# Kernel optimization log

Hardware: AMD Instinct MI355X
Metric: run time of the kernel (lower is better)

Reference implementation:

```python
import jax, jax.numpy as jnp
import numpy as np

N_NODES = 4096
EDGE_PROB = 0.01


def setup_inputs() -> dict:
    key = jax.random.key(0)
    kx, ka, kw = jax.random.split(key, 3)
    x = jax.random.normal(kx, (4, 32, N_NODES, 12), dtype=jnp.float32)
    u = jax.random.uniform(ka, (N_NODES, N_NODES), dtype=jnp.float32)
    adj = (u < EDGE_PROB).astype(jnp.float32)
    adj = jnp.maximum(adj, adj.T)
    weight = jax.random.normal(kw, (3, 32, 32), dtype=jnp.float32) * 0.1
    bias = jnp.zeros((32,), dtype=jnp.float32)
    return {"x": x, "adj": adj, "weight": weight, "bias": bias}


def reference(x, adj, weight, bias):
    # x: [B, c_in, N, T] -> [B, T, N, c_in] as in AdaptiveGraphConv.forward
    B, C, N, T = x.shape
    h = jnp.transpose(x, (0, 3, 2, 1))  # [B, T, N, C]
    # DenseChebConv (K=3): L = I - D^{-1/2} A D^{-1/2}, inf -> 0 for isolated nodes
    d = adj.sum(axis=-1)
    d_inv_sqrt = jnp.where(d > 0, jnp.where(d > 0, d, 1.0) ** -0.5, 0.0)
    norm_adj = d_inv_sqrt[:, None] * adj * d_inv_sqrt[None, :]
    L = jnp.eye(N, dtype=x.dtype) - norm_adj
    Tx0 = h
    Tx1 = jnp.einsum('mn,btnc->btmc', L, h)
    Tx2 = 2.0 * jnp.einsum('mn,btnc->btmc', L, Tx1) - Tx0
    out = (jnp.einsum('btnc,co->btno', Tx0, weight[0])
           + jnp.einsum('btnc,co->btno', Tx1, weight[1])
           + jnp.einsum('btnc,co->btno', Tx2, weight[2])
           + bias)
    # back to [B, c_out, N, T]
    return jnp.transpose(out, (0, 3, 2, 1))
```

## Files before the change

### kernel.cpp

```cpp
#include <hip/hip_runtime.h>

#define NN 4096
#define CC 32
#define TT 12
#define BB 4
#define BT 48
#define NC 1536
#define MAXD 192
#define FW 512
#define NCH 3
#define STP 36
#define SOP 33

typedef float f32x4 __attribute__((ext_vector_type(4)));
typedef short short8 __attribute__((ext_vector_type(8)));
typedef unsigned short ushort8 __attribute__((ext_vector_type(8)));

__device__ __forceinline__ float bf2f(unsigned short h) {
  return __uint_as_float(((unsigned int)h) << 16);
}
__device__ __forceinline__ unsigned short f2bf(float f) {
  unsigned int u = __float_as_uint(f);
  return (unsigned short)((u + 0x7FFFu + ((u >> 16) & 1u)) >> 16);
}
__device__ __forceinline__ float blo(unsigned int w) { return __uint_as_float(w << 16); }
__device__ __forceinline__ float bhi(unsigned int w) { return __uint_as_float(w & 0xFFFF0000u); }

__global__ __launch_bounds__(256) void k_build(const float* __restrict__ adj,
                                               uint2* __restrict__ edges,
                                               int* __restrict__ deg, float* __restrict__ dis) {
  __shared__ int cnt;
  int m = blockIdx.x;
  if (threadIdx.x == 0) cnt = 0;
  __syncthreads();
  unsigned int* ecol = (unsigned int*)(edges + m * MAXD);
  const uint4* row = (const uint4*)(adj + (size_t)m * NN);
  for (int i = threadIdx.x; i < NN / 4; i += 256) {
    uint4 v = row[i];
    unsigned int ws[4] = {v.x, v.y, v.z, v.w};
    #pragma unroll
    for (int k = 0; k < 4; ++k) {
      if (ws[k] != 0) {
        int p = atomicAdd(&cnt, 1);
        if (p < MAXD) ecol[p * 2] = (unsigned int)(i * 4 + k);
      }
    }
  }
  __syncthreads();
  if (threadIdx.x == 0) {
    int d = cnt < MAXD ? cnt : MAXD;
    deg[m] = d;
    dis[m] = d > 0 ? (float)(1.0 / sqrt((double)d)) : 0.0f;
  }
}

__global__ __launch_bounds__(192) void k_wt(uint2* __restrict__ edges,
                                            const int* __restrict__ deg,
                                            int* __restrict__ degp,
                                            const float* __restrict__ dis) {
  int m = blockIdx.x;
  int j = threadIdx.x;
  int d = deg[m];
  int dp = (d + 15) & ~15;
  if (j < d) {
    unsigned int* e = (unsigned int*)(edges + m * MAXD + j);
    e[1] = __float_as_uint(dis[e[0]]);
  } else if (j < dp) {
    edges[m * MAXD + j] = make_uint2((unsigned int)m, 0u);
  }
  if (j == 0) degp[m] = dp;
}

__global__ __launch_bounds__(256) void k_trans(const float* __restrict__ x,
                                               unsigned short* __restrict__ H) {
  __shared__ unsigned short sT[192 * STP];
  int b = blockIdx.x >> 8;
  int n0 = (blockIdx.x & 255) * 16;
  int c = threadIdx.x >> 3;
  int l8 = threadIdx.x & 7;
  size_t base = ((size_t)(b * CC + c) * NN + n0) * TT;
  #pragma unroll
  for (int it = 0; it < 6; ++it) {
    int j0 = it * 32 + l8 * 4;
    float4 f = *(const float4*)(x + base + j0);
    sT[(j0 + 0) * STP + c] = f2bf(f.x);
    sT[(j0 + 1) * STP + c] = f2bf(f.y);
    sT[(j0 + 2) * STP + c] = f2bf(f.z);
    sT[(j0 + 3) * STP + c] = f2bf(f.w);
  }
  __syncthreads();
  #pragma unroll
  for (int k = 0; k < 6; ++k) {
    int p = (threadIdx.x >> 3) + 32 * k;
    int nl = p / TT, t = p - nl * TT;
    ushort4 v = *(const ushort4*)&sT[p * STP + l8 * 4];
    size_t off = ((size_t)(n0 + nl) * BT + b * TT + t) * CC + l8 * 4;
    *(ushort4*)(H + off) = v;
  }
}

__global__ __launch_bounds__(256) void k_gather(const unsigned short* __restrict__ S,
                                                const uint2* __restrict__ edges,
                                                const int* __restrict__ degp,
                                                const float* __restrict__ dis,
                                                unsigned short* __restrict__ D) {
  int wid = __builtin_amdgcn_readfirstlane(threadIdx.x >> 6);
  int lane = threadIdx.x & 63;
  int m = blockIdx.x * 4 + wid;
  int d = degp[m];
  float dm = dis[m];
  const uint2* ep = edges + m * MAXD;
  int fo = blockIdx.y * FW + lane * 8;
  const unsigned short* Sf = S + fo;
  float a0 = 0.f, a1 = 0.f, a2 = 0.f, a3 = 0.f;
  float a4 = 0.f, a5 = 0.f, a6 = 0.f, a7 = 0.f;
  for (int e = 0; e < d; e += 8) {
    uint4 hv[8];
    float w[8];
    #pragma unroll
    for (int k = 0; k < 8; ++k) {
      uint2 ew = ep[e + k];
      w[k] = __uint_as_float(ew.y);
      hv[k] = *(const uint4*)(Sf + (int)ew.x * NC);
    }
    #pragma unroll
    for (int k = 0; k < 8; ++k) {
      float wk = w[k];
      a0 = fmaf(wk, blo(hv[k].x), a0); a1 = fmaf(wk, bhi(hv[k].x), a1);
      a2 = fmaf(wk, blo(hv[k].y), a2); a3 = fmaf(wk, bhi(hv[k].y), a3);
      a4 = fmaf(wk, blo(hv[k].z), a4); a5 = fmaf(wk, bhi(hv[k].z), a5);
      a6 = fmaf(wk, blo(hv[k].w), a6); a7 = fmaf(wk, bhi(hv[k].w), a7);
    }
  }
  ushort8 o;
  o[0] = f2bf(dm * a0); o[1] = f2bf(dm * a1);
  o[2] = f2bf(dm * a2); o[3] = f2bf(dm * a3);
  o[4] = f2bf(dm * a4); o[5] = f2bf(dm * a5);
  o[6] = f2bf(dm * a6); o[7] = f2bf(dm * a7);
  *(ushort8*)(D + (size_t)m * NC + fo) = o;
}

__global__ __launch_bounds__(256) void k_mix(const unsigned short* __restrict__ H,
                                             const unsigned short* __restrict__ G1,
                                             const unsigned short* __restrict__ G2,
                                             const float* __restrict__ W,
                                             const float* __restrict__ bias,
                                             float* __restrict__ out) {
  __shared__ __align__(16) float sOut[192 * SOP];
  int wid = threadIdx.x >> 6, lane = threadIdx.x & 63;
  int lm = lane & 15, quad = lane >> 4;
  short8 bhf[2][3], blf[2][3];
  float bias0[2];
  for (int h = 0; h < 2; ++h)
    for (int g = 0; g < 3; ++g) {
      short8 vh, vl;
      #pragma unroll
      for (int j = 0; j < 8; ++j) {
        int r = quad * 8 + j, c = h * 16 + lm;
        float w0 = W[(0 * CC + r) * CC + c];
        float w1 = W[(1 * CC + r) * CC + c];
        float w2 = W[(2 * CC + r) * CC + c];
        float w = (g == 0) ? (w0 + w1 + w2)
                 : (g == 1) ? (-w1 - 4.f * w2)
                            : (2.f * w2);
        unsigned short hi = f2bf(w);
        vh[j] = (short)hi;
        vl[j] = (short)f2bf(w - bf2f(hi));
      }
      bhf[h][g] = vh; blf[h][g] = vl;
    }
  #pragma unroll
  for (int h = 0; h < 2; ++h) bias0[h] = bias[h * 16 + lm];
  int n0 = blockIdx.x * 4;
  #pragma unroll
  for (int tI = 0; tI < 3; ++tI) {
    int r0l = wid * BT + tI * 16;
    size_t abase = ((size_t)(n0 * BT) + r0l + lm) * CC + quad * 8;
    short8 af0 = *(const short8*)(H + abase);
    short8 af1 = *(const short8*)(G1 + abase);
    short8 af2 = *(const short8*)(G2 + abase);
    #pragma unroll
    for (int h = 0; h < 2; ++h) {
      f32x4 acc = {bias0[h], bias0[h], bias0[h], bias0[h]};
      acc = __builtin_amdgcn_mfma_f32_16x16x32_bf16(af0, bhf[h][0], acc, 0, 0, 0);
      acc = __builtin_amdgcn_mfma_f32_16x16x32_bf16(af0, blf[h][0], acc, 0, 0, 0);
      acc = __builtin_amdgcn_mfma_f32_16x16x32_bf16(af1, bhf[h][1], acc, 0, 0, 0);
      acc = __builtin_amdgcn_mfma_f32_16x16x32_bf16(af1, blf[h][1], acc, 0, 0, 0);
      acc = __builtin_amdgcn_mfma_f32_16x16x32_bf16(af2, bhf[h][2], acc, 0, 0, 0);
      acc = __builtin_amdgcn_mfma_f32_16x16x32_bf16(af2, blf[h][2], acc, 0, 0, 0);
      int o = h * 16 + lm;
      #pragma unroll
      for (int reg = 0; reg < 4; ++reg)
        sOut[(r0l + quad * 4 + reg) * SOP + o] = acc[reg];
    }
  }
  __syncthreads();
  #pragma unroll
  for (int j = 0; j < 6; ++j) {
    int idx = j * 256 + threadIdx.x;
    int bo = idx / 12;
    int fq = idx - bo * 12;
    int p0 = fq * 4;
    float v[4];
    #pragma unroll
    for (int k = 0; k < 4; ++k) {
      int p = p0 + k;
      int nl = p / TT, t = p - nl * TT;
      int b = bo >> 5, o = bo & 31;
      v[k] = sOut[(nl * BT + b * TT + t) * SOP + o];
    }
    size_t base = (((size_t)bo * NN) + n0) * TT + p0;
    *(float4*)(out + base) = make_float4(v[0], v[1], v[2], v[3]);
  }
}

extern "C" void kernel_launch(void* const* d_in, const int* in_sizes, int n_in,
                              void* d_out, int out_size, void* d_ws, size_t ws_size,
                              hipStream_t stream) {
  const float* x    = (const float*)d_in[0];
  const float* adj  = (const float*)d_in[1];
  const float* wgt  = (const float*)d_in[2];
  const float* bias = (const float*)d_in[3];
  char* ws = (char*)d_ws;
  float* dis  = (float*)ws;
  int*   deg  = (int*)(ws + 16384);
  int*   degp = (int*)(ws + 32768);
  uint2* edges = (uint2*)(ws + 49152);
  char* p = ws + 49152 + (size_t)NN * MAXD * 8;
  unsigned short* H  = (unsigned short*)p;
  unsigned short* G1 = (unsigned short*)(p + (size_t)NN * NC * 2);
  unsigned short* G2 = (unsigned short*)(p + (size_t)NN * NC * 4);

  k_build<<<NN, 256, 0, stream>>>(adj, edges, deg, dis);
  k_wt<<<NN, 192, 0, stream>>>(edges, deg, degp, dis);
  k_trans<<<1024, 256, 0, stream>>>(x, H);
  k_gather<<<dim3(NN / 4, NCH), 256, 0, stream>>>(H, edges, degp, dis, G1);
  k_gather<<<dim3(NN / 4, NCH), 256, 0, stream>>>(G1, edges, degp, dis, G2);
  k_mix<<<NN / 4, 256, 0, stream>>>(H, G1, G2, wgt, bias, (float*)d_out);
}
```

Before: 241.0 us.

## Stage gather loads through LDS with direct global-to-LDS async loads

The sparse gather kernel now uses global_load_lds to copy each group of 8 neighbor feature rows straight into per-wave shared memory. It reads the current group from LDS while the next group's loads are in flight, giving a two-stage software pipeline in place of register-held loads. This is meant to hide gather latency and cut register pressure. It adds LDS usage and explicit waitcnt/sched barriers. It also assumes the degree is padded to a multiple of 8, so any remainder is dropped if padding is absent.

```diff
diff --git a/kernel.cpp b/kernel.cpp
--- a/kernel.cpp
+++ b/kernel.cpp
@@ -9,12 +9,16 @@
 #define MAXD 192
 #define FW 512
 #define NCH 3
+#define GRP 8
 #define STP 36
 #define SOP 33
 
 typedef float f32x4 __attribute__((ext_vector_type(4)));
 typedef short short8 __attribute__((ext_vector_type(8)));
 typedef unsigned short ushort8 __attribute__((ext_vector_type(8)));
+
+typedef __attribute__((address_space(3))) unsigned int lds_u32;
+typedef __attribute__((address_space(1))) const unsigned int glb_u32;
 
 __device__ __forceinline__ float bf2f(unsigned short h) {
   return __uint_as_float(((unsigned int)h) << 16);
@@ -104,34 +108,55 @@
                                                 const int* __restrict__ degp,
                                                 const float* __restrict__ dis,
                                                 unsigned short* __restrict__ D) {
-  int wid = __builtin_amdgcn_readfirstlane(threadIdx.x >> 6);
-  int lane = threadIdx.x & 63;
+  __shared__ __align__(16) unsigned short sb[4][GRP][FW];
+  int tid = threadIdx.x;
+  int wid = __builtin_amdgcn_readfirstlane(tid >> 6);
+  int lane = tid & 63;
   int m = blockIdx.x * 4 + wid;
   int d = degp[m];
   float dm = dis[m];
-  const uint2* ep = edges + m * MAXD;
-  int fo = blockIdx.y * FW + lane * 8;
-  const unsigned short* Sf = S + fo;
+  const uint2* ep = edges + (size_t)m * MAXD;
+  const unsigned short* Sy = S + blockIdx.y * FW + lane * 8;
   float a0 = 0.f, a1 = 0.f, a2 = 0.f, a3 = 0.f;
   float a4 = 0.f, a5 = 0.f, a6 = 0.f, a7 = 0.f;
-  for (int e = 0; e < d; e += 8) {
-    uint4 hv[8];
-    float w[8];
-    #pragma unroll
-    for (int k = 0; k < 8; ++k) {
-      uint2 ew = ep[e + k];
-      w[k] = __uint_as_float(ew.y);
-      hv[k] = *(const uint4*)(Sf + (int)ew.x * NC);
-    }
-    #pragma unroll
-    for (int k = 0; k < 8; ++k) {
-      float wk = w[k];
-      a0 = fmaf(wk, blo(hv[k].x), a0); a1 = fmaf(wk, bhi(hv[k].x), a1);
-      a2 = fmaf(wk, blo(hv[k].y), a2); a3 = fmaf(wk, bhi(hv[k].y), a3);
-      a4 = fmaf(wk, blo(hv[k].z), a4); a5 = fmaf(wk, bhi(hv[k].z), a5);
-      a6 = fmaf(wk, blo(hv[k].w), a6); a7 = fmaf(wk, bhi(hv[k].w), a7);
-    }
-  }
+
+  auto ISSUE = [&](int g) {
+    #pragma unroll
+    for (int k = 0; k < GRP; ++k) {
+      uint2 ew = ep[g * GRP + k];
+      __builtin_amdgcn_global_load_lds((glb_u32*)(Sy + (int)ew.x * NC),
+                                       (lds_u32*)&sb[wid][k][0], 16, 0, 0);
+    }
+  };
+
+  if (d) {
+    int ng = d >> 3;
+    ISSUE(0);
+    for (int g = 0; g < ng; ++g) {
+      asm volatile("s_waitcnt vmcnt(0)" ::: "memory");
+      __builtin_amdgcn_sched_barrier(0);
+      uint4 v[GRP];
+      float w[GRP];
+      #pragma unroll
+      for (int k = 0; k < GRP; ++k) {
+        v[k] = *(const uint4*)&sb[wid][k][lane * 8];
+        w[k] = __uint_as_float(ep[g * GRP + k].y);
+      }
+      asm volatile("s_waitcnt lgkmcnt(0)" ::: "memory");
+      __builtin_amdgcn_sched_barrier(0);
+      if (g + 1 < ng) ISSUE(g + 1);
+      __builtin_amdgcn_sched_barrier(0);
+      #pragma unroll
+      for (int k = 0; k < GRP; ++k) {
+        float wk = w[k];
+        a0 = fmaf(wk, blo(v[k].x), a0); a1 = fmaf(wk, bhi(v[k].x), a1);
+        a2 = fmaf(wk, blo(v[k].y), a2); a3 = fmaf(wk, bhi(v[k].y), a3);
+        a4 = fmaf(wk, blo(v[k].z), a4); a5 = fmaf(wk, bhi(v[k].z), a5);
+        a6 = fmaf(wk, blo(v[k].w), a6); a7 = fmaf(wk, bhi(v[k].w), a7);
+      }
+    }
+  }
+  int fo = blockIdx.y * FW + lane * 8;
   ushort8 o;
   o[0] = f2bf(dm * a0); o[1] = f2bf(dm * a1);
   o[2] = f2bf(dm * a2); o[3] = f2bf(dm * a3);
```

Result: no change. 245.0 us (+1.7%).
